# Performance work log

Hardware: AMD Instinct MI355X
Metric: run time of the kernel (lower is better)

## Reference

```python
import jax, jax.numpy as jnp
import numpy as np

N_QUBITS = 4
N_LAYERS = 2


def _apply_1q(state, U, wire):
    # state: (M,) + (2,)*n complex64; U: (2,2) shared or (M,2,2) per-sample
    s = jnp.moveaxis(state, 1 + wire, -1)
    if U.ndim == 2:
        s = jnp.einsum('...i,ji->...j', s, U)
    else:
        s = jnp.einsum('m...i,mji->m...j', s, U)
    return jnp.moveaxis(s, -1, 1 + wire)


def _apply_cnot(state, c, t):
    # flip target axis on the control=1 subspace
    s = jnp.moveaxis(state, (1 + c, 1 + t), (1, 2))
    s = jnp.stack([s[:, 0], s[:, 1, ::-1]], axis=1)
    return jnp.moveaxis(s, (1, 2), (1 + c, 1 + t))


def _rx(theta):
    # theta: (M,) -> (M,2,2); RX = [[cos, -i sin], [-i sin, cos]] of theta/2
    c = jnp.cos(theta / 2).astype(jnp.complex64)
    s = ((-1j) * jnp.sin(theta / 2)).astype(jnp.complex64)
    return jnp.stack([jnp.stack([c, s], -1), jnp.stack([s, c], -1)], -2)


def _rot(phi, theta, omega):
    # Rot = RZ(omega) RY(theta) RZ(phi)
    c = jnp.cos(theta / 2)
    s = jnp.sin(theta / 2)
    ep = jnp.exp(-0.5j * (phi + omega))
    em = jnp.exp(0.5j * (phi - omega))
    row0 = jnp.stack([ep * c, -em * s])
    row1 = jnp.stack([jnp.conj(em) * s, jnp.conj(ep) * c])
    return jnp.stack([row0, row1]).astype(jnp.complex64)


def _circuit(xf, weights):
    # xf: (M, n) angles; weights: (L, n, 3)
    M, n = xf.shape
    state = jnp.zeros((M, 2 ** n), jnp.complex64).at[:, 0].set(1.0)
    state = state.reshape((M,) + (2,) * n)
    # AngleEmbedding (RX per wire, per-sample angles)
    for w in range(n):
        state = _apply_1q(state, _rx(xf[:, w]), w)
    # StronglyEntanglingLayers
    for l in range(N_LAYERS):
        for w in range(n):
            state = _apply_1q(state, _rot(weights[l, w, 0], weights[l, w, 1], weights[l, w, 2]), w)
        r = l % (n - 1) + 1  # default PennyLane ranges
        for w in range(n):
            state = _apply_cnot(state, w, (w + r) % n)
    # expval PauliZ(0) = p(wire0=0) - p(wire0=1)
    probs = (state.real ** 2 + state.imag ** 2).reshape(M, 2, -1)
    return probs[:, 0].sum(-1) - probs[:, 1].sum(-1)


def setup_inputs() -> dict:
    key = jax.random.key(0)
    k1, k2 = jax.random.split(key)
    x = jax.random.normal(k1, (64, 8192, N_QUBITS), dtype=jnp.float32)
    weights = jax.random.uniform(k2, (N_LAYERS, N_QUBITS, 3), dtype=jnp.float32,
                                 minval=0.0, maxval=2.0 * np.pi)
    return {"x": x, "weights": weights}


def reference(x, weights):
    B, N, n = x.shape
    out = _circuit(x.reshape(-1, n), weights)
    return out.reshape(B, N, 1).astype(jnp.float32)
```

## Files before the change

kernel.cpp:

```cpp
#include <hip/hip_runtime.h>


#define SPT 4

struct c32 { float x, y; };
__device__ inline c32 cmul(c32 a, c32 b) { return { a.x*b.x - a.y*b.y, a.x*b.y + a.y*b.x }; }
__device__ inline c32 cadd(c32 a, c32 b) { return { a.x + b.x, a.y + b.y }; }

__global__ __launch_bounds__(256) void qq_fused(const float4* __restrict__ x,
                                                const float* __restrict__ wgt,
                                                float* __restrict__ out, int M) {
    __shared__ float trigC[24], trigS[24];
    __shared__ c32 V[16][16];
    __shared__ c32 Mm[16][16];
    __shared__ float As[81];
    const int tid = threadIdx.x;

    if (tid < 24) {
        const int g = tid / 3, sel = tid - 3 * g;
        const float phi = wgt[g * 3 + 0], th = wgt[g * 3 + 1], om = wgt[g * 3 + 2];
        const float ang = (sel == 0) ? 0.5f * th
                        : (sel == 1) ? 0.5f * (phi + om)
                                     : 0.5f * (phi - om);
        __sincosf(ang, &trigS[tid], &trigC[tid]);
    }
    __syncthreads();

    if (tid < 16) {
        c32 st[16];
#pragma unroll
        for (int k = 0; k < 16; ++k) st[k] = { 0.f, 0.f };
        st[tid] = { 1.f, 0.f };

#pragma unroll
        for (int l = 0; l < 2; ++l) {
#pragma unroll
            for (int wi = 0; wi < 4; ++wi) {
                const int g = l * 4 + wi;
                const float ct = trigC[3 * g],     sth = trigS[3 * g];
                const float cp = trigC[3 * g + 1], sp  = trigS[3 * g + 1];
                const float cm = trigC[3 * g + 2], sm  = trigS[3 * g + 2];
                const c32 U00 = {  cp * ct,  -sp * ct  };
                const c32 U01 = { -cm * sth, -sm * sth };
                const c32 U10 = {  cm * sth, -sm * sth };
                const c32 U11 = {  cp * ct,   sp * ct  };
                const int bit = 8 >> wi;
#pragma unroll
                for (int b = 0; b < 16; ++b) {
                    if (!(b & bit)) {
                        const c32 a0 = st[b], a1 = st[b | bit];
                        st[b]       = cadd(cmul(U00, a0), cmul(U01, a1));
                        st[b | bit] = cadd(cmul(U10, a0), cmul(U11, a1));
                    }
                }
            }
            const int r = (l == 0) ? 1 : 2;
#pragma unroll
            for (int wi = 0; wi < 4; ++wi) {
                const int cbit = 8 >> wi;
                const int tbit = 8 >> ((wi + r) & 3);
#pragma unroll
                for (int b = 0; b < 16; ++b) {
                    if ((b & cbit) && !(b & tbit)) {
                        const c32 tmp = st[b];
                        st[b] = st[b | tbit];
                        st[b | tbit] = tmp;
                    }
                }
            }
        }
#pragma unroll
        for (int k = 0; k < 16; ++k) V[k][tid] = st[k];
    }
    __syncthreads();

    {
        const int i = tid >> 4, j = tid & 15;
        c32 acc = { 0.f, 0.f };
#pragma unroll
        for (int k = 0; k < 16; ++k) {
            const float z = (k & 8) ? -1.f : 1.f;
            const c32 vi = V[k][i], vj = V[k][j];
            acc.x += z * (vi.x * vj.x + vi.y * vj.y);
            acc.y += z * (vi.x * vj.y - vi.y * vj.x);
        }
        Mm[i][j] = acc;
    }
    __syncthreads();

    if (tid < 81) {
        const int t = tid;
        const int tw[4] = { t / 27, (t / 9) % 3, (t / 3) % 3, t % 3 };
        int maskY = 0, maskZY = 0, nY = 0;
#pragma unroll
        for (int w = 0; w < 4; ++w) {
            const int bit = 8 >> w;
            if (tw[w] == 2) { maskY |= bit; ++nY; }
            if (tw[w] != 0) maskZY |= bit;
        }
        float sx = 0.f, sy = 0.f;
#pragma unroll
        for (int i = 0; i < 16; ++i) {
            const float sgn = (__popc(i & maskZY) & 1) ? -1.f : 1.f;
            const c32 m = Mm[i][i ^ maskY];
            sx += sgn * m.x;
            sy += sgn * m.y;
        }
        float re;
        switch (nY & 3) {
            case 0:  re =  sx; break;
            case 1:  re = -sy; break;
            case 2:  re = -sx; break;
            default: re =  sy; break;
        }
        As[t] = re * (1.f / 16.f);
    }
    __syncthreads();

    const int base = blockIdx.x * (256 * SPT) + tid;
    float4 xv[SPT];
#pragma unroll
    for (int s = 0; s < SPT; ++s) {
        const int idx = base + s * 256;
        xv[s] = (idx < M) ? x[idx] : make_float4(0.f, 0.f, 0.f, 0.f);
    }
    float c0[SPT], y0[SPT], c1[SPT], y1[SPT], c2[SPT], y2[SPT], c3[SPT], y3[SPT];
#pragma unroll
    for (int s = 0; s < SPT; ++s) {
        float sn;
        __sincosf(xv[s].x, &sn, &c0[s]); y0[s] = -sn;
        __sincosf(xv[s].y, &sn, &c1[s]); y1[s] = -sn;
        __sincosf(xv[s].z, &sn, &c2[s]); y2[s] = -sn;
        __sincosf(xv[s].w, &sn, &c3[s]); y3[s] = -sn;
    }

    float lvl0[SPT][3];
#pragma unroll
    for (int t0 = 0; t0 < 3; ++t0) {
        float lvl1[SPT][3];
#pragma unroll
        for (int t1 = 0; t1 < 3; ++t1) {
            float v[SPT][3];
#pragma unroll
            for (int t2 = 0; t2 < 3; ++t2) {
                const int b = ((t0 * 3 + t1) * 3 + t2) * 3;
                const float a0 = As[b], a1 = As[b + 1], a2 = As[b + 2];
#pragma unroll
                for (int s = 0; s < SPT; ++s)
                    v[s][t2] = fmaf(y3[s], a2, fmaf(c3[s], a1, a0));
            }
#pragma unroll
            for (int s = 0; s < SPT; ++s)
                lvl1[s][t1] = fmaf(y2[s], v[s][2], fmaf(c2[s], v[s][1], v[s][0]));
        }
#pragma unroll
        for (int s = 0; s < SPT; ++s)
            lvl0[s][t0] = fmaf(y1[s], lvl1[s][2], fmaf(c1[s], lvl1[s][1], lvl1[s][0]));
    }
#pragma unroll
    for (int s = 0; s < SPT; ++s) {
        const int idx = base + s * 256;
        if (idx < M)
            out[idx] = fmaf(y0[s], lvl0[s][2], fmaf(c0[s], lvl0[s][1], lvl0[s][0]));
    }
}

extern "C" void kernel_launch(void* const* d_in, const int* in_sizes, int n_in,
                              void* d_out, int out_size, void* d_ws, size_t ws_size,
                              hipStream_t stream) {
    const float* x = (const float*)d_in[0];
    const float* w = (const float*)d_in[1];
    const int M = in_sizes[0] / 4;
    const int blocks = (M + 256 * SPT - 1) / (256 * SPT);
    qq_fused<<<blocks, 256, 0, stream>>>((const float4*)x, w, (float*)d_out, M);
}
```

Before: 68.95 us.

## Parallelize per-block unitary build across all threads and prefetch inputs early

The 16x16 circuit unitary was previously built by 16 threads, each holding a full 16-amplitude column. It is now built by all 256 threads, one amplitude each, with gates applied through wavefront xor-shuffles. Gate matrices are precomputed once into shared memory by 8 threads. The global loads of x are issued before the prologue so their latency overlaps the setup work. The shuffle approach relies on each 16-lane group sitting inside one wavefront, which holds for 64-wide wavefronts. Loading early keeps the loaded values live across the setup, which may raise register pressure.

```diff
diff --git a/kernel.cpp b/kernel.cpp
--- a/kernel.cpp
+++ b/kernel.cpp
@@ -4,87 +4,83 @@
 #define SPT 4
 
 struct c32 { float x, y; };
-__device__ inline c32 cmul(c32 a, c32 b) { return { a.x*b.x - a.y*b.y, a.x*b.y + a.y*b.x }; }
-__device__ inline c32 cadd(c32 a, c32 b) { return { a.x + b.x, a.y + b.y }; }
 
 __global__ __launch_bounds__(256) void qq_fused(const float4* __restrict__ x,
                                                 const float* __restrict__ wgt,
                                                 float* __restrict__ out, int M) {
-    __shared__ float trigC[24], trigS[24];
+    __shared__ float Ug[8][8];
     __shared__ c32 V[16][16];
     __shared__ c32 Mm[16][16];
     __shared__ float As[81];
     const int tid = threadIdx.x;
 
-    if (tid < 24) {
-        const int g = tid / 3, sel = tid - 3 * g;
-        const float phi = wgt[g * 3 + 0], th = wgt[g * 3 + 1], om = wgt[g * 3 + 2];
-        const float ang = (sel == 0) ? 0.5f * th
-                        : (sel == 1) ? 0.5f * (phi + om)
-                                     : 0.5f * (phi - om);
-        __sincosf(ang, &trigS[tid], &trigC[tid]);
+    const int base = blockIdx.x * (256 * SPT) + tid;
+    float4 xv[SPT];
+#pragma unroll
+    for (int s = 0; s < SPT; ++s) {
+        const int idx = base + s * 256;
+        xv[s] = (idx < M) ? x[idx] : make_float4(0.f, 0.f, 0.f, 0.f);
+    }
+
+    if (tid < 8) {
+        const float* wp = wgt + tid * 3;
+        const float phi = wp[0], th = wp[1], om = wp[2];
+        float ct, sth, cp, sp, cm, sm;
+        __sincosf(0.5f * th, &sth, &ct);
+        __sincosf(0.5f * (phi + om), &sp, &cp);
+        __sincosf(0.5f * (phi - om), &sm, &cm);
+        Ug[tid][0] =  cp * ct;  Ug[tid][1] = -sp * ct;
+        Ug[tid][2] = -cm * sth; Ug[tid][3] = -sm * sth;
+        Ug[tid][4] =  cm * sth; Ug[tid][5] = -sm * sth;
+        Ug[tid][6] =  cp * ct;  Ug[tid][7] =  sp * ct;
     }
     __syncthreads();
 
-    if (tid < 16) {
-        c32 st[16];
-#pragma unroll
-        for (int k = 0; k < 16; ++k) st[k] = { 0.f, 0.f };
-        st[tid] = { 1.f, 0.f };
-
+    {
+        const int k = tid & 15;
+        float ar = (k == (tid >> 4)) ? 1.f : 0.f, ai = 0.f;
 #pragma unroll
         for (int l = 0; l < 2; ++l) {
 #pragma unroll
             for (int wi = 0; wi < 4; ++wi) {
-                const int g = l * 4 + wi;
-                const float ct = trigC[3 * g],     sth = trigS[3 * g];
-                const float cp = trigC[3 * g + 1], sp  = trigS[3 * g + 1];
-                const float cm = trigC[3 * g + 2], sm  = trigS[3 * g + 2];
-                const c32 U00 = {  cp * ct,  -sp * ct  };
-                const c32 U01 = { -cm * sth, -sm * sth };
-                const c32 U10 = {  cm * sth, -sm * sth };
-                const c32 U11 = {  cp * ct,   sp * ct  };
-                const int bit = 8 >> wi;
-#pragma unroll
-                for (int b = 0; b < 16; ++b) {
-                    if (!(b & bit)) {
-                        const c32 a0 = st[b], a1 = st[b | bit];
-                        st[b]       = cadd(cmul(U00, a0), cmul(U01, a1));
-                        st[b | bit] = cadd(cmul(U10, a0), cmul(U11, a1));
-                    }
-                }
+                const int g = l * 4 + wi, bit = 8 >> wi;
+                const float u00r = Ug[g][0], u00i = Ug[g][1];
+                const float u01r = Ug[g][2], u01i = Ug[g][3];
+                const float u10r = Ug[g][4], u10i = Ug[g][5];
+                const float u11r = Ug[g][6], u11i = Ug[g][7];
+                const float pr = __shfl_xor(ar, bit);
+                const float pi = __shfl_xor(ai, bit);
+                const bool hi = (k & bit) != 0;
+                const float uar = hi ? u11r : u00r, uai = hi ? u11i : u00i;
+                const float upr = hi ? u10r : u01r, upi = hi ? u10i : u01i;
+                const float nr = uar * ar - uai * ai + upr * pr - upi * pi;
+                const float ni = uar * ai + uai * ar + upr * pi + upi * pr;
+                ar = nr; ai = ni;
             }
-            const int r = (l == 0) ? 1 : 2;
+            const int r = l ? 2 : 1;
 #pragma unroll
             for (int wi = 0; wi < 4; ++wi) {
-                const int cbit = 8 >> wi;
-                const int tbit = 8 >> ((wi + r) & 3);
-#pragma unroll
-                for (int b = 0; b < 16; ++b) {
-                    if ((b & cbit) && !(b & tbit)) {
-                        const c32 tmp = st[b];
-                        st[b] = st[b | tbit];
-                        st[b | tbit] = tmp;
-                    }
-                }
+                const int cbit = 8 >> wi, tbit = 8 >> ((wi + r) & 3);
+                const float pr = __shfl_xor(ar, tbit);
+                const float pi = __shfl_xor(ai, tbit);
+                if (k & cbit) { ar = pr; ai = pi; }
             }
         }
-#pragma unroll
-        for (int k = 0; k < 16; ++k) V[k][tid] = st[k];
+        V[k][tid >> 4] = { ar, ai };
     }
     __syncthreads();
 
     {
         const int i = tid >> 4, j = tid & 15;
-        c32 acc = { 0.f, 0.f };
+        float accx = 0.f, accy = 0.f;
 #pragma unroll
         for (int k = 0; k < 16; ++k) {
             const float z = (k & 8) ? -1.f : 1.f;
             const c32 vi = V[k][i], vj = V[k][j];
-            acc.x += z * (vi.x * vj.x + vi.y * vj.y);
-            acc.y += z * (vi.x * vj.y - vi.y * vj.x);
+            accx += z * (vi.x * vj.x + vi.y * vj.y);
+            accy += z * (vi.x * vj.y - vi.y * vj.x);
         }
-        Mm[i][j] = acc;
+        Mm[i][j] = { accx, accy };
     }
     __syncthreads();
 
@@ -117,13 +113,6 @@
     }
     __syncthreads();
 
-    const int base = blockIdx.x * (256 * SPT) + tid;
-    float4 xv[SPT];
-#pragma unroll
-    for (int s = 0; s < SPT; ++s) {
-        const int idx = base + s * 256;
-        xv[s] = (idx < M) ? x[idx] : make_float4(0.f, 0.f, 0.f, 0.f);
-    }
     float c0[SPT], y0[SPT], c1[SPT], y1[SPT], c2[SPT], y2[SPT], c3[SPT], y3[SPT];
 #pragma unroll
     for (int s = 0; s < SPT; ++s) {
```

Measured after the change: 62.70 us. 1.1x faster.
